# Optimization experiments

Hardware: AMD Instinct MI355X
Metric: run time of the kernel (lower is better)

## Reference

```python
import jax, jax.numpy as jnp
import numpy as np

N = 8192
F_IN = 512
F_OUT = 64
ALPHA = 0.2  # LeakyReLU negative slope
MASK_VAL = -9e15


def setup_inputs() -> dict:
    key = jax.random.key(0)
    k1, k2, k3, k4, k5 = jax.random.split(key, 5)
    x = jax.random.normal(k1, (N, F_IN), dtype=jnp.float32)
    adj = jax.random.randint(k2, (N, N), 0, 2, dtype=jnp.int32)
    # params: W uniform(-stdv, stdv) per reset_parameters, A xavier-ish
    stdv = 1.0 / np.sqrt(F_OUT)
    W = jax.random.uniform(k3, (F_IN, F_OUT), dtype=jnp.float32, minval=-stdv, maxval=stdv)
    bias = jax.random.uniform(k4, (F_OUT,), dtype=jnp.float32, minval=-stdv, maxval=stdv)
    A = jax.random.normal(k5, (2 * F_OUT, 1), dtype=jnp.float32) * 0.1
    return {"x": x, "adj": adj, "W": W, "bias": bias, "A": A}


def reference(x, adj, W, bias, A):
    # Wh: [N, F_OUT]
    Wh = x @ W
    # e_ij = leakyrelu([Wh_i || Wh_j] @ A) == leakyrelu(Wh_i @ a1 + Wh_j @ a2)
    # (mathematically identical to the N x N x 2F concat, without materializing it)
    a1 = A[:F_OUT, 0]  # [F_OUT]
    a2 = A[F_OUT:, 0]  # [F_OUT]
    s1 = Wh @ a1  # [N]
    s2 = Wh @ a2  # [N]
    e = jax.nn.leaky_relu(s1[:, None] + s2[None, :], negative_slope=ALPHA)  # [N, N]
    masked = jnp.where(adj > 0, e, MASK_VAL)
    attention = jax.nn.softmax(masked, axis=1)  # [N, N]
    # dropout p=0.0 -> identity
    out = attention @ Wh + bias  # [N, F_OUT]
    return out
```

## Files before the change

kernel.cpp:

```cpp
#include <hip/hip_runtime.h>

#define NN 8192
#define FIN 512
#define FOUT 64
#define LRELU_ALPHA 0.2f
#define LOG2E 1.4426950408889634f

typedef __attribute__((ext_vector_type(4))) float f32x4;
typedef __attribute__((ext_vector_type(4))) int i32x4;
typedef __attribute__((ext_vector_type(8))) __bf16 bf16x8;
typedef __attribute__((ext_vector_type(4))) __bf16 bf16x4;

#if __has_builtin(__builtin_amdgcn_exp2f)
#define EXP2F(x) __builtin_amdgcn_exp2f(x)
#else
#define EXP2F(x) exp2f(x)
#endif

__global__ __launch_bounds__(256) void gat_wh(
    const float* __restrict__ x, const float* __restrict__ W,
    const float* __restrict__ A,
    __bf16* __restrict__ WhbT, float* __restrict__ s1, float* __restrict__ s2)
{
    const int wid  = (blockIdx.x * 256 + threadIdx.x) >> 6;
    const int lane = threadIdx.x & 63;
    const int cg   = lane & 15;
    const int kh   = lane >> 4;
    const int row0 = wid * 4;

    f32x4 acc[4];
    #pragma unroll
    for (int r_ = 0; r_ < 4; ++r_) acc[r_] = (f32x4){0.f, 0.f, 0.f, 0.f};

    const float* xb   = x + (size_t)row0 * FIN + kh * 128;
    const float* wcol = W + cg * 4 + (size_t)kh * 128 * FOUT;

    #pragma unroll 2
    for (int k = 0; k < 128; k += 4) {
        f32x4 wv[4];
        #pragma unroll
        for (int u = 0; u < 4; ++u)
            wv[u] = *reinterpret_cast<const f32x4*>(wcol + (size_t)(k + u) * FOUT);
        #pragma unroll
        for (int r_ = 0; r_ < 4; ++r_) {
            f32x4 xv = *reinterpret_cast<const f32x4*>(xb + (size_t)r_ * FIN + k);
            acc[r_] += xv[0] * wv[0];
            acc[r_] += xv[1] * wv[1];
            acc[r_] += xv[2] * wv[2];
            acc[r_] += xv[3] * wv[3];
        }
    }

    #pragma unroll
    for (int r_ = 0; r_ < 4; ++r_) {
        #pragma unroll
        for (int u = 0; u < 4; ++u) {
            acc[r_][u] += __shfl_xor(acc[r_][u], 16);
            acc[r_][u] += __shfl_xor(acc[r_][u], 32);
        }
    }

    f32x4 a1v = *reinterpret_cast<const f32x4*>(A + cg * 4);
    f32x4 a2v = *reinterpret_cast<const f32x4*>(A + FOUT + cg * 4);
    #pragma unroll
    for (int r_ = 0; r_ < 4; ++r_) {
        float s1p = acc[r_][0]*a1v[0] + acc[r_][1]*a1v[1] + acc[r_][2]*a1v[2] + acc[r_][3]*a1v[3];
        float s2p = acc[r_][0]*a2v[0] + acc[r_][1]*a2v[1] + acc[r_][2]*a2v[2] + acc[r_][3]*a2v[3];
        #pragma unroll
        for (int off = 1; off < 16; off <<= 1) {
            s1p += __shfl_xor(s1p, off);
            s2p += __shfl_xor(s2p, off);
        }
        if (lane == 0) { s1[row0 + r_] = s1p; s2[row0 + r_] = s2p; }
    }

    if (kh == 0) {
        #pragma unroll
        for (int u = 0; u < 4; ++u) {
            bf16x4 pk;
            pk[0] = (__bf16)acc[0][u];
            pk[1] = (__bf16)acc[1][u];
            pk[2] = (__bf16)acc[2][u];
            pk[3] = (__bf16)acc[3][u];
            *reinterpret_cast<bf16x4*>(WhbT + (size_t)(cg * 4 + u) * NN + row0) = pk;
        }
    }
}

__global__ __launch_bounds__(256) void gat_attn(
    const int* __restrict__ adj, const __bf16* __restrict__ WhbT,
    const float* __restrict__ s1g, const float* __restrict__ s2g,
    const float* __restrict__ bias, float* __restrict__ out)
{
    __shared__ float s2l[NN];
    __shared__ float red[4];
    __shared__ float ol[4][16];
    __shared__ float oacc[4][16][FOUT];

    const int tid  = threadIdx.x;
    const int w    = tid >> 6;
    const int lane = tid & 63;
    const int r    = lane & 15;
    const int q    = lane >> 4;
    const int row0 = blockIdx.x * 16;

    float mx = -3.0e38f;
    for (int i = tid; i < NN / 4; i += 256) {
        f32x4 v = reinterpret_cast<const f32x4*>(s2g)[i];
        v *= LOG2E;
        reinterpret_cast<f32x4*>(s2l)[i] = v;
        mx = fmaxf(mx, fmaxf(fmaxf(v[0], v[1]), fmaxf(v[2], v[3])));
    }
    #pragma unroll
    for (int off = 1; off < 64; off <<= 1)
        mx = fmaxf(mx, __shfl_xor(mx, off));
    if (lane == 0) red[w] = mx;
    __syncthreads();
    const float s2maxl = fmaxf(fmaxf(red[0], red[1]), fmaxf(red[2], red[3]));

    const float s1l = s1g[row0 + r] * LOG2E;
    const float tM  = s1l + s2maxl;
    const float Ml  = fmaxf(tM, LRELU_ALPHA * tM);
    const float c1  = s1l - Ml;
    const float c2  = LRELU_ALPHA * s1l - Ml;

    float l = 0.f;
    f32x4 acc0 = {0,0,0,0}, acc1 = {0,0,0,0}, acc2 = {0,0,0,0}, acc3 = {0,0,0,0};

    const int*    adjp = adj + (size_t)(row0 + r) * NN + q * 8;
    const __bf16* wp   = WhbT + q * 8;
    const float*  s2b_ = s2l + q * 8;

    for (int it = 0; it < 32; ++it) {
        const int j0 = (w << 11) + (it << 6);
        #pragma unroll
        for (int c = 0; c < 2; ++c) {
            const int jc = j0 + (c << 5);
            i32x4 av0 = *reinterpret_cast<const i32x4*>(adjp + jc);
            i32x4 av1 = *reinterpret_cast<const i32x4*>(adjp + jc + 4);
            bf16x8 b0 = *reinterpret_cast<const bf16x8*>(wp + (size_t)(0 * 16 + r) * NN + jc);
            bf16x8 b1 = *reinterpret_cast<const bf16x8*>(wp + (size_t)(1 * 16 + r) * NN + jc);
            bf16x8 b2 = *reinterpret_cast<const bf16x8*>(wp + (size_t)(2 * 16 + r) * NN + jc);
            bf16x8 b3 = *reinterpret_cast<const bf16x8*>(wp + (size_t)(3 * 16 + r) * NN + jc);
            f32x4 s2a = *reinterpret_cast<const f32x4*>(s2b_ + jc);
            f32x4 s2c = *reinterpret_cast<const f32x4*>(s2b_ + jc + 4);

            bf16x8 af;
            float ps = 0.f;
            #pragma unroll
            for (int i = 0; i < 4; ++i) {
                float g0 = fmaxf(c1 + s2a[i], fmaf(LRELU_ALPHA, s2a[i], c2));
                g0 = (av0[i] > 0) ? g0 : -3.0e38f;
                float p0 = EXP2F(g0);
                ps += p0;
                af[i] = (__bf16)p0;
                float g1 = fmaxf(c1 + s2c[i], fmaf(LRELU_ALPHA, s2c[i], c2));
                g1 = (av1[i] > 0) ? g1 : -3.0e38f;
                float p1 = EXP2F(g1);
                ps += p1;
                af[i + 4] = (__bf16)p1;
            }
            l += ps;
            acc0 = __builtin_amdgcn_mfma_f32_16x16x32_bf16(af, b0, acc0, 0, 0, 0);
            acc1 = __builtin_amdgcn_mfma_f32_16x16x32_bf16(af, b1, acc1, 0, 0, 0);
            acc2 = __builtin_amdgcn_mfma_f32_16x16x32_bf16(af, b2, acc2, 0, 0, 0);
            acc3 = __builtin_amdgcn_mfma_f32_16x16x32_bf16(af, b3, acc3, 0, 0, 0);
        }
    }

    l += __shfl_xor(l, 16);
    l += __shfl_xor(l, 32);
    if (lane < 16) ol[w][lane] = l;
    #pragma unroll
    for (int reg = 0; reg < 4; ++reg) {
        oacc[w][q * 4 + reg][0 * 16 + r] = acc0[reg];
        oacc[w][q * 4 + reg][1 * 16 + r] = acc1[reg];
        oacc[w][q * 4 + reg][2 * 16 + r] = acc2[reg];
        oacc[w][q * 4 + reg][3 * 16 + r] = acc3[reg];
    }
    __syncthreads();

    for (int o = tid; o < 16 * FOUT; o += 256) {
        const int rr = o >> 6;
        const int f  = o & 63;
        const float L = ol[0][rr] + ol[1][rr] + ol[2][rr] + ol[3][rr];
        const float O = oacc[0][rr][f] + oacc[1][rr][f] + oacc[2][rr][f] + oacc[3][rr][f];
        out[(size_t)(row0 + rr) * FOUT + f] = O / L + bias[f];
    }
}

extern "C" void kernel_launch(void* const* d_in, const int* in_sizes, int n_in,
                              void* d_out, int out_size, void* d_ws, size_t ws_size,
                              hipStream_t stream)
{
    const float* x    = (const float*)d_in[0];
    const int*   adj  = (const int*)d_in[1];
    const float* W    = (const float*)d_in[2];
    const float* bias = (const float*)d_in[3];
    const float* A    = (const float*)d_in[4];
    float* out = (float*)d_out;

    char* ws = (char*)d_ws;
    __bf16* WhbT = (__bf16*)ws;
    float*  s1   = (float*)(ws + (size_t)FOUT * NN * sizeof(__bf16));
    float*  s2   = s1 + NN;

    gat_wh<<<dim3(512), dim3(256), 0, stream>>>(x, W, A, WhbT, s1, s2);
    gat_attn<<<dim3(NN / 16), dim3(256), 0, stream>>>(adj, WhbT, s1, s2, bias, out);
}
```

Baseline: 409.2 us.

## Stage adjacency tiles through LDS for coalesced loads and precompute scaled s2

Each wave now loads 16 rows by 128 columns of the int32 adjacency matrix with contiguous 512-byte row segments into a per-wave LDS tile, then reads its MFMA operand fragments from LDS. Previously each lane read small strided pieces across 16 different rows. The log2e-scaled s2 vector is computed once in the first kernel and read from global memory instead of being copied into a 32KB LDS array per block. This is meant to improve DRAM coalescing on the dominant adjacency stream, at the cost of extra LDS traffic and reliance on intra-wave ordering without a barrier.

```diff
diff --git a/kernel.cpp b/kernel.cpp
--- a/kernel.cpp
+++ b/kernel.cpp
@@ -5,6 +5,7 @@
 #define FOUT 64
 #define LRELU_ALPHA 0.2f
 #define LOG2E 1.4426950408889634f
+#define TS 132
 
 typedef __attribute__((ext_vector_type(4))) float f32x4;
 typedef __attribute__((ext_vector_type(4))) int i32x4;
@@ -20,7 +21,8 @@
 __global__ __launch_bounds__(256) void gat_wh(
     const float* __restrict__ x, const float* __restrict__ W,
     const float* __restrict__ A,
-    __bf16* __restrict__ WhbT, float* __restrict__ s1, float* __restrict__ s2)
+    __bf16* __restrict__ WhbT, float* __restrict__ s1, float* __restrict__ s2,
+    float* __restrict__ s2log)
 {
     const int wid  = (blockIdx.x * 256 + threadIdx.x) >> 6;
     const int lane = threadIdx.x & 63;
@@ -71,7 +73,11 @@
             s1p += __shfl_xor(s1p, off);
             s2p += __shfl_xor(s2p, off);
         }
-        if (lane == 0) { s1[row0 + r_] = s1p; s2[row0 + r_] = s2p; }
+        if (lane == 0) {
+            s1[row0 + r_] = s1p;
+            s2[row0 + r_] = s2p;
+            s2log[row0 + r_] = s2p * LOG2E;
+        }
     }
 
     if (kh == 0) {
@@ -89,10 +95,10 @@
 
 __global__ __launch_bounds__(256) void gat_attn(
     const int* __restrict__ adj, const __bf16* __restrict__ WhbT,
-    const float* __restrict__ s1g, const float* __restrict__ s2g,
+    const float* __restrict__ s1g, const float* __restrict__ s2log,
     const float* __restrict__ bias, float* __restrict__ out)
 {
-    __shared__ float s2l[NN];
+    __shared__ int  adjt[4][16][TS];
     __shared__ float red[4];
     __shared__ float ol[4][16];
     __shared__ float oacc[4][16][FOUT];
@@ -106,9 +112,7 @@
 
     float mx = -3.0e38f;
     for (int i = tid; i < NN / 4; i += 256) {
-        f32x4 v = reinterpret_cast<const f32x4*>(s2g)[i];
-        v *= LOG2E;
-        reinterpret_cast<f32x4*>(s2l)[i] = v;
+        f32x4 v = reinterpret_cast<const f32x4*>(s2log)[i];
         mx = fmaxf(mx, fmaxf(fmaxf(v[0], v[1]), fmaxf(v[2], v[3])));
     }
     #pragma unroll
@@ -127,23 +131,37 @@
     float l = 0.f;
     f32x4 acc0 = {0,0,0,0}, acc1 = {0,0,0,0}, acc2 = {0,0,0,0}, acc3 = {0,0,0,0};
 
-    const int*    adjp = adj + (size_t)(row0 + r) * NN + q * 8;
-    const __bf16* wp   = WhbT + q * 8;
-    const float*  s2b_ = s2l + q * 8;
-
-    for (int it = 0; it < 32; ++it) {
-        const int j0 = (w << 11) + (it << 6);
-        #pragma unroll
-        for (int c = 0; c < 2; ++c) {
-            const int jc = j0 + (c << 5);
-            i32x4 av0 = *reinterpret_cast<const i32x4*>(adjp + jc);
-            i32x4 av1 = *reinterpret_cast<const i32x4*>(adjp + jc + 4);
-            bf16x8 b0 = *reinterpret_cast<const bf16x8*>(wp + (size_t)(0 * 16 + r) * NN + jc);
-            bf16x8 b1 = *reinterpret_cast<const bf16x8*>(wp + (size_t)(1 * 16 + r) * NN + jc);
-            bf16x8 b2 = *reinterpret_cast<const bf16x8*>(wp + (size_t)(2 * 16 + r) * NN + jc);
-            bf16x8 b3 = *reinterpret_cast<const bf16x8*>(wp + (size_t)(3 * 16 + r) * NN + jc);
-            f32x4 s2a = *reinterpret_cast<const f32x4*>(s2b_ + jc);
-            f32x4 s2c = *reinterpret_cast<const f32x4*>(s2b_ + jc + 4);
+    const int srow  = lane >> 5;
+    const int scol  = (lane & 31) << 2;
+    const int* adjs = adj + (size_t)(row0 + srow) * NN + (w << 11) + scol;
+
+    const __bf16* wpb  = WhbT + (w << 11) + (q << 3);
+    const __bf16* wp0  = wpb + (size_t)(0 * 16 + r) * NN;
+    const __bf16* wp1  = wpb + (size_t)(1 * 16 + r) * NN;
+    const __bf16* wp2  = wpb + (size_t)(2 * 16 + r) * NN;
+    const __bf16* wp3  = wpb + (size_t)(3 * 16 + r) * NN;
+    const float*  s2p_ = s2log + (w << 11) + (q << 3);
+
+    for (int it = 0; it < 16; ++it) {
+        const int c0 = it << 7;
+
+        #pragma unroll
+        for (int i = 0; i < 8; ++i) {
+            i32x4 v = *reinterpret_cast<const i32x4*>(adjs + (size_t)(2 * i) * NN + c0);
+            *reinterpret_cast<i32x4*>(&adjt[w][2 * i + srow][scol]) = v;
+        }
+
+        #pragma unroll
+        for (int h = 0; h < 4; ++h) {
+            const int jc = c0 + (h << 5);
+            i32x4 av0 = *reinterpret_cast<const i32x4*>(&adjt[w][r][(h << 5) + (q << 3)]);
+            i32x4 av1 = *reinterpret_cast<const i32x4*>(&adjt[w][r][(h << 5) + (q << 3) + 4]);
+            bf16x8 b0 = *reinterpret_cast<const bf16x8*>(wp0 + jc);
+            bf16x8 b1 = *reinterpret_cast<const bf16x8*>(wp1 + jc);
+            bf16x8 b2 = *reinterpret_cast<const bf16x8*>(wp2 + jc);
+            bf16x8 b3 = *reinterpret_cast<const bf16x8*>(wp3 + jc);
+            f32x4 s2a = *reinterpret_cast<const f32x4*>(s2p_ + jc);
+            f32x4 s2c = *reinterpret_cast<const f32x4*>(s2p_ + jc + 4);
 
             bf16x8 af;
             float ps = 0.f;
@@ -173,10 +191,10 @@
     if (lane < 16) ol[w][lane] = l;
     #pragma unroll
     for (int reg = 0; reg < 4; ++reg) {
-        oacc[w][q * 4 + reg][0 * 16 + r] = acc0[reg];
-        oacc[w][q * 4 + reg][1 * 16 + r] = acc1[reg];
-        oacc[w][q * 4 + reg][2 * 16 + r] = acc2[reg];
-        oacc[w][q * 4 + reg][3 * 16 + r] = acc3[reg];
+        oacc[w][(q << 2) + reg][0 * 16 + r] = acc0[reg];
+        oacc[w][(q << 2) + reg][1 * 16 + r] = acc1[reg];
+        oacc[w][(q << 2) + reg][2 * 16 + r] = acc2[reg];
+        oacc[w][(q << 2) + reg][3 * 16 + r] = acc3[reg];
     }
     __syncthreads();
 
@@ -201,10 +219,11 @@
     float* out = (float*)d_out;
 
     char* ws = (char*)d_ws;
-    __bf16* WhbT = (__bf16*)ws;
-    float*  s1   = (float*)(ws + (size_t)FOUT * NN * sizeof(__bf16));
-    float*  s2   = s1 + NN;
-
-    gat_wh<<<dim3(512), dim3(256), 0, stream>>>(x, W, A, WhbT, s1, s2);
-    gat_attn<<<dim3(NN / 16), dim3(256), 0, stream>>>(adj, WhbT, s1, s2, bias, out);
+    __bf16* WhbT  = (__bf16*)ws;
+    float*  s1    = (float*)(ws + (size_t)FOUT * NN * sizeof(__bf16));
+    float*  s2    = s1 + NN;
+    float*  s2log = s2 + NN;
+
+    gat_wh<<<dim3(512), dim3(256), 0, stream>>>(x, W, A, WhbT, s1, s2, s2log);
+    gat_attn<<<dim3(NN / 16), dim3(256), 0, stream>>>(adj, WhbT, s1, s2log, bias, out);
 }
```

After: 452.8 us. 1.11x slower.
